# Kernel tuning notes

Hardware: AMD Instinct MI355X
Metric: run time of the kernel (lower is better)

The kernel has to match this reference:

```python
import jax, jax.numpy as jnp
import numpy as np

N_CLASSES_FG = 20  # n_classes - 1

def _norm(t, axis=1):
    # F.normalize(t, dim=axis, eps=1e-10)
    n = jnp.linalg.norm(t, axis=axis, keepdims=True)
    return t / jnp.maximum(n, 1e-10)

def setup_inputs() -> dict:
    key = jax.random.key(0)
    ks = jax.random.split(key, 6)
    B, C, H, W = 8, 512, 80, 80
    N, Hr, Wr = 100, 40, 40
    return {
        "code_C": jax.random.normal(ks[0], (B, C, H, W), jnp.float32),
        "code_BG": jax.random.normal(ks[1], (B, C, H, W), jnp.float32),
        "ref_code_c": jax.random.normal(ks[2], (N, C, Hr, Wr), jnp.float32),
        "ref_code_bg": jax.random.normal(ks[3], (N, C, Hr, Wr), jnp.float32),
        "sum_patch_coord": jax.random.randint(ks[4], (N, 2), 0, Hr, dtype=jnp.int32),
        "cls_mask": jax.random.randint(ks[5], (N,), 0, N_CLASSES_FG, dtype=jnp.int32),
    }

def reference(code_C, code_BG, ref_code_c, ref_code_bg, sum_patch_coord, cls_mask):
    B, Cdim, H, W = code_C.shape
    N = ref_code_c.shape[0]
    code_C = _norm(code_C)   # channelwise L2 normalize
    code_BG = _norm(code_BG)
    # gather per-annotation feature vectors: ref_code_c[i, :, pc[i,1], pc[i,0]] -> [N, C]
    code_vectors = ref_code_c[jnp.arange(N), :, sum_patch_coord[:, 1], sum_patch_coord[:, 0]]
    # mean-mode prototypes: class-wise mean of gathered vectors
    protos = jax.ops.segment_sum(code_vectors, cls_mask, num_segments=N_CLASSES_FG)  # [V, C]
    counts = jax.ops.segment_sum(jnp.ones((N,), code_vectors.dtype), cls_mask, num_segments=N_CLASSES_FG)
    protos = protos / jnp.maximum(counts, 1.0)[:, None]  # classes with 0 vectors stay zero
    # cosine-similarity maps against normalized prototypes
    prob_C = jnp.einsum('bchw,vc->bvhw', code_C, _norm(protos, axis=1))  # [B, V, H, W]
    # pick the most-background pixel (min of summed class similarity), k=1 topk(-x)
    flat = prob_C.sum(axis=1).reshape(B, -1)  # [B, H*W]
    idx = jnp.argmin(flat, axis=1)
    i_x, i_y = idx // W, idx % W
    min_vec = code_BG[jnp.arange(B), :, i_x, i_y]  # [B, C]
    prob_BG = jnp.einsum('bchw,bc->bhw', code_BG, min_vec)  # [B, H, W]
    probs = jnp.concatenate([prob_BG[:, None], prob_C], axis=1)  # [B, V+1, H, W]
    return jax.nn.softmax(probs, axis=1)
```

## Files before the change

### kernel.cpp

```cpp
#include <hip/hip_runtime.h>
#include <math.h>

#define BB 8
#define CC 512
#define HWSZ 6400
#define NN 100
#define HR 40
#define WR 40
#define VV 20
#define VO 21
#define TPX 256
#define NT (HWSZ / TPX)

typedef unsigned long long u64;

__device__ __forceinline__ unsigned mapf(float f) {
    unsigned b = __float_as_uint(f);
    return (b & 0x80000000u) ? ~b : (b | 0x80000000u);
}

__global__ __launch_bounds__(512) void k_protos(const float* __restrict__ refc,
                                                const int* __restrict__ coord,
                                                const int* __restrict__ cls,
                                                float* __restrict__ protosT,
                                                u64* __restrict__ batchMin) {
    const int v = blockIdx.x;
    const int c = threadIdx.x;
    if (v == 0 && c < BB) batchMin[c] = ~0ull;

    float acc = 0.f;
    int cnt = 0;
    for (int n = 0; n < NN; ++n) {
        if (cls[n] == v) {
            int y = coord[2 * n + 1];
            int x = coord[2 * n + 0];
            acc += refc[((size_t)(n * CC + c) * HR + y) * WR + x];
            ++cnt;
        }
    }
    acc /= fmaxf((float)cnt, 1.0f);

    float ss = acc * acc;
    #pragma unroll
    for (int off = 32; off; off >>= 1) ss += __shfl_xor(ss, off);
    __shared__ float sW[8];
    const int wave = c >> 6, lane = c & 63;
    if (lane == 0) sW[wave] = ss;
    __syncthreads();
    float tot = 0.f;
    #pragma unroll
    for (int w = 0; w < 8; ++w) tot += sW[w];
    float scale = 1.0f / fmaxf(sqrtf(tot), 1e-10f);

    protosT[c * VV + v] = acc * scale;
}

__global__ __launch_bounds__(256) void k_probC_part(const float* __restrict__ codeC,
                                                    const float* __restrict__ protosT,
                                                    float* __restrict__ partC) {
    __shared__ float red[4 * 11 * TPX];

    const int tid  = threadIdx.x;
    const int w    = tid >> 6, lane = tid & 63;
    const int blk  = blockIdx.x;
    const int cg   = blk & 1;
    const int tile = (blk >> 1) % NT;
    const int b    = blk / (2 * NT);
    const int c0   = __builtin_amdgcn_readfirstlane(cg * 256 + w * 64);

    const float* src = codeC + ((size_t)(b * CC + c0)) * HWSZ + tile * TPX + 4 * lane;
    const float* pt  = protosT + (size_t)c0 * VV;

    float4 d[VV];
    #pragma unroll
    for (int v = 0; v < VV; ++v) d[v] = make_float4(0.f, 0.f, 0.f, 0.f);
    float4 ss = make_float4(0.f, 0.f, 0.f, 0.f);

    #pragma unroll 8
    for (int c = 0; c < 64; ++c) {
        float4 x = *(const float4*)(src + (size_t)c * HWSZ);
        ss.x = fmaf(x.x, x.x, ss.x);
        ss.y = fmaf(x.y, x.y, ss.y);
        ss.z = fmaf(x.z, x.z, ss.z);
        ss.w = fmaf(x.w, x.w, ss.w);
        const float* pr = pt + c * VV;
        #pragma unroll
        for (int v = 0; v < VV; ++v) {
            float p = pr[v];
            d[v].x = fmaf(x.x, p, d[v].x);
            d[v].y = fmaf(x.y, p, d[v].y);
            d[v].z = fmaf(x.z, p, d[v].z);
            d[v].w = fmaf(x.w, p, d[v].w);
        }
    }

    float* dstp = partC + (size_t)blk * (VO * TPX);

    *(float4*)&red[(w * 11 + 0) * TPX + 4 * lane] = ss;
    #pragma unroll
    for (int r = 0; r < 10; ++r)
        *(float4*)&red[(w * 11 + 1 + r) * TPX + 4 * lane] = d[r];
    __syncthreads();
    for (int q = tid; q < 11 * TPX; q += 256) {
        float t = red[q] + red[11 * TPX + q] + red[22 * TPX + q] + red[33 * TPX + q];
        dstp[q] = t;
    }
    __syncthreads();

    #pragma unroll
    for (int r = 0; r < 10; ++r)
        *(float4*)&red[(w * 11 + r) * TPX + 4 * lane] = d[10 + r];
    __syncthreads();
    for (int q = tid; q < 10 * TPX; q += 256) {
        float t = red[q] + red[11 * TPX + q] + red[22 * TPX + q] + red[33 * TPX + q];
        dstp[11 * TPX + q] = t;
    }
}

__global__ __launch_bounds__(256) void k_finishC(const float* __restrict__ partC,
                                                 float* __restrict__ probC,
                                                 u64* __restrict__ batchMin) {
    __shared__ u64 sKey[4];
    const int tid  = threadIdx.x;
    const int tile = blockIdx.x % NT;
    const int b    = blockIdx.x / NT;

    const float* p0 = partC + ((size_t)(b * 2 * NT + tile * 2)) * (VO * TPX);
    const float* p1 = p0 + VO * TPX;

    float ssT = p0[tid] + p1[tid];
    float scale = 1.0f / fmaxf(sqrtf(ssT), 1e-10f);

    float psum = 0.f;
    float* dst = probC + (size_t)b * VV * HWSZ + tile * TPX;
    #pragma unroll
    for (int v = 0; v < VV; ++v) {
        float dv = p0[(1 + v) * TPX + tid] + p1[(1 + v) * TPX + tid];
        float pv = dv * scale;
        dst[(size_t)v * HWSZ + tid] = pv;
        psum += pv;
    }

    u64 key = ((u64)mapf(psum) << 32) | (unsigned)(tile * TPX + tid);
    #pragma unroll
    for (int off = 32; off; off >>= 1) {
        u64 o = __shfl_xor(key, off);
        if (o < key) key = o;
    }
    if ((tid & 63) == 0) sKey[tid >> 6] = key;
    __syncthreads();
    if (tid == 0) {
        u64 kk = sKey[0];
        kk = sKey[1] < kk ? sKey[1] : kk;
        kk = sKey[2] < kk ? sKey[2] : kk;
        kk = sKey[3] < kk ? sKey[3] : kk;
        atomicMin(&batchMin[b], kk);
    }
}

__global__ __launch_bounds__(512) void k_minvec(const u64* __restrict__ batchMin,
                                                const float* __restrict__ codeBG,
                                                float* __restrict__ minvecN) {
    const int b = blockIdx.x, c = threadIdx.x;
    const int pix = (int)(unsigned)(batchMin[b] & 0xFFFFFFFFull);
    float x = codeBG[(size_t)(b * CC + c) * HWSZ + pix];
    float ss = x * x;
    #pragma unroll
    for (int off = 32; off; off >>= 1) ss += __shfl_xor(ss, off);
    __shared__ float sW[8];
    if ((c & 63) == 0) sW[c >> 6] = ss;
    __syncthreads();
    float tot = 0.f;
    #pragma unroll
    for (int w = 0; w < 8; ++w) tot += sW[w];
    minvecN[b * CC + c] = x * (1.0f / fmaxf(sqrtf(tot), 1e-10f));
}

__global__ __launch_bounds__(256) void k_bg_part(const float* __restrict__ codeBG,
                                                 const float* __restrict__ minvecN,
                                                 float* __restrict__ partBG) {
    __shared__ float red[4 * 2 * TPX];

    const int tid  = threadIdx.x;
    const int w    = tid >> 6, lane = tid & 63;
    const int blk  = blockIdx.x;
    const int cg   = blk & 1;
    const int tile = (blk >> 1) % NT;
    const int b    = blk / (2 * NT);
    const int c0   = __builtin_amdgcn_readfirstlane(cg * 256 + w * 64);

    const float* src = codeBG + ((size_t)(b * CC + c0)) * HWSZ + tile * TPX + 4 * lane;
    const float* mv  = minvecN + b * CC + c0;

    float4 ss = make_float4(0.f, 0.f, 0.f, 0.f);
    float4 dg = make_float4(0.f, 0.f, 0.f, 0.f);

    #pragma unroll 8
    for (int c = 0; c < 64; ++c) {
        float4 x = *(const float4*)(src + (size_t)c * HWSZ);
        float m = mv[c];
        ss.x = fmaf(x.x, x.x, ss.x);
        ss.y = fmaf(x.y, x.y, ss.y);
        ss.z = fmaf(x.z, x.z, ss.z);
        ss.w = fmaf(x.w, x.w, ss.w);
        dg.x = fmaf(x.x, m, dg.x);
        dg.y = fmaf(x.y, m, dg.y);
        dg.z = fmaf(x.z, m, dg.z);
        dg.w = fmaf(x.w, m, dg.w);
    }

    *(float4*)&red[(w * 2 + 0) * TPX + 4 * lane] = ss;
    *(float4*)&red[(w * 2 + 1) * TPX + 4 * lane] = dg;
    __syncthreads();

    float* dstp = partBG + (size_t)blk * (2 * TPX);
    for (int q = tid; q < 2 * TPX; q += 256) {
        float t = red[q] + red[2 * TPX + q] + red[4 * TPX + q] + red[6 * TPX + q];
        dstp[q] = t;
    }
}

__global__ __launch_bounds__(256) void k_finishBG(const float* __restrict__ partBG,
                                                  const float* __restrict__ probC,
                                                  float* __restrict__ out) {
    const int tid  = threadIdx.x;
    const int tile = blockIdx.x % NT;
    const int b    = blockIdx.x / NT;

    const float* q0 = partBG + ((size_t)(b * 2 * NT + tile * 2)) * (2 * TPX);
    const float* q1 = q0 + 2 * TPX;

    float ssT = q0[tid] + q1[tid];
    float dgT = q0[TPX + tid] + q1[TPX + tid];
    float pbg = dgT * (1.0f / fmaxf(sqrtf(ssT), 1e-10f));

    float pv[VO];
    pv[0] = pbg;
    const float* pc = probC + (size_t)b * VV * HWSZ + tile * TPX + tid;
    #pragma unroll
    for (int v = 0; v < VV; ++v) pv[v + 1] = pc[(size_t)v * HWSZ];

    float m = pv[0];
    #pragma unroll
    for (int i = 1; i < VO; ++i) m = fmaxf(m, pv[i]);
    float se = 0.f;
    #pragma unroll
    for (int i = 0; i < VO; ++i) { pv[i] = __expf(pv[i] - m); se += pv[i]; }
    float inv = 1.0f / se;

    float* dstp = out + (size_t)b * VO * HWSZ + tile * TPX + tid;
    #pragma unroll
    for (int i = 0; i < VO; ++i) dstp[(size_t)i * HWSZ] = pv[i] * inv;
}

extern "C" void kernel_launch(void* const* d_in, const int* in_sizes, int n_in,
                              void* d_out, int out_size, void* d_ws, size_t ws_size,
                              hipStream_t stream) {
    const float* codeC  = (const float*)d_in[0];
    const float* codeBG = (const float*)d_in[1];
    const float* refc   = (const float*)d_in[2];
    const int* coord = (const int*)d_in[4];
    const int* cls   = (const int*)d_in[5];
    float* out = (float*)d_out;

    char* ws = (char*)d_ws;
    float* protosT  = (float*)(ws);
    float* probC    = (float*)(ws + 40960);
    float* minvecN  = (float*)(ws + 4136960);
    u64*   batchMin = (u64*)  (ws + 4153344);
    float* partC    = (float*)(ws + 4153408);
    float* partBG   = (float*)(ws + 12755008);

    k_protos    <<<dim3(VV),          dim3(512), 0, stream>>>(refc, coord, cls, protosT, batchMin);
    k_probC_part<<<dim3(BB * NT * 2), dim3(256), 0, stream>>>(codeC, protosT, partC);
    k_finishC   <<<dim3(BB * NT),     dim3(256), 0, stream>>>(partC, probC, batchMin);
    k_minvec    <<<dim3(BB),          dim3(512), 0, stream>>>(batchMin, codeBG, minvecN);
    k_bg_part   <<<dim3(BB * NT * 2), dim3(256), 0, stream>>>(codeBG, minvecN, partBG);
    k_finishBG  <<<dim3(BB * NT),     dim3(256), 0, stream>>>(partBG, probC, out);
}
```

Before: 67.60 us.

## Fuse finish stages into partial kernels via last-block atomic counters

Merges the six launches into three. The last of the two channel-group blocks per tile finishes the tile, and the last tile per batch computes the normalized min vector, all coordinated through atomic counters and thread fences. This removes launch gaps and the separate small kernels that run at low occupancy. In exchange it adds fences, atomics and serialized tail work inside the big kernels, and the counters must be reset by k_protos on each call.

```diff
diff --git a/kernel.cpp b/kernel.cpp
--- a/kernel.cpp
+++ b/kernel.cpp
@@ -23,10 +23,16 @@
                                                 const int* __restrict__ coord,
                                                 const int* __restrict__ cls,
                                                 float* __restrict__ protosT,
-                                                u64* __restrict__ batchMin) {
+                                                u64* __restrict__ batchMin,
+                                                unsigned* __restrict__ tileCntA,
+                                                unsigned* __restrict__ tileCntB,
+                                                unsigned* __restrict__ batchCnt) {
     const int v = blockIdx.x;
     const int c = threadIdx.x;
-    if (v == 0 && c < BB) batchMin[c] = ~0ull;
+    if (v == 0) {
+        if (c < BB * NT) { tileCntA[c] = 0u; tileCntB[c] = 0u; }
+        if (c < BB) { batchCnt[c] = 0u; batchMin[c] = ~0ull; }
+    }
 
     float acc = 0.f;
     int cnt = 0;
@@ -55,10 +61,20 @@
     protosT[c * VV + v] = acc * scale;
 }
 
-__global__ __launch_bounds__(256) void k_probC_part(const float* __restrict__ codeC,
-                                                    const float* __restrict__ protosT,
-                                                    float* __restrict__ partC) {
+__global__ __launch_bounds__(256) void k_probC(const float* __restrict__ codeC,
+                                               const float* __restrict__ codeBG,
+                                               const float* __restrict__ protosT,
+                                               float* __restrict__ partC,
+                                               float* __restrict__ probC,
+                                               u64* __restrict__ batchMin,
+                                               unsigned* __restrict__ tileCntA,
+                                               unsigned* __restrict__ batchCnt,
+                                               float* __restrict__ minvecN) {
     __shared__ float red[4 * 11 * TPX];
+    __shared__ u64 sKey[4];
+    __shared__ int sLast, sBLast;
+    __shared__ unsigned sPix;
+    __shared__ float sR[4];
 
     const int tid  = threadIdx.x;
     const int w    = tid >> 6, lane = tid & 63;
@@ -115,22 +131,21 @@
         float t = red[q] + red[11 * TPX + q] + red[22 * TPX + q] + red[33 * TPX + q];
         dstp[11 * TPX + q] = t;
     }
-}
-
-__global__ __launch_bounds__(256) void k_finishC(const float* __restrict__ partC,
-                                                 float* __restrict__ probC,
-                                                 u64* __restrict__ batchMin) {
-    __shared__ u64 sKey[4];
-    const int tid  = threadIdx.x;
-    const int tile = blockIdx.x % NT;
-    const int b    = blockIdx.x / NT;
-
-    const float* p0 = partC + ((size_t)(b * 2 * NT + tile * 2)) * (VO * TPX);
+
+    __threadfence();
+    if (tid == 0) {
+        unsigned old = atomicAdd(&tileCntA[b * NT + tile], 1u);
+        sLast = (old == 1u) ? 1 : 0;
+    }
+    __syncthreads();
+    if (!sLast) return;
+    __threadfence();
+
+    const float* p0 = partC + (size_t)(b * 2 * NT + tile * 2) * (VO * TPX);
     const float* p1 = p0 + VO * TPX;
 
     float ssT = p0[tid] + p1[tid];
     float scale = 1.0f / fmaxf(sqrtf(ssT), 1e-10f);
-
     float psum = 0.f;
     float* dst = probC + (size_t)b * VV * HWSZ + tile * TPX;
     #pragma unroll
@@ -147,7 +162,7 @@
         u64 o = __shfl_xor(key, off);
         if (o < key) key = o;
     }
-    if ((tid & 63) == 0) sKey[tid >> 6] = key;
+    if (lane == 0) sKey[w] = key;
     __syncthreads();
     if (tid == 0) {
         u64 kk = sKey[0];
@@ -155,31 +170,41 @@
         kk = sKey[2] < kk ? sKey[2] : kk;
         kk = sKey[3] < kk ? sKey[3] : kk;
         atomicMin(&batchMin[b], kk);
-    }
-}
-
-__global__ __launch_bounds__(512) void k_minvec(const u64* __restrict__ batchMin,
-                                                const float* __restrict__ codeBG,
-                                                float* __restrict__ minvecN) {
-    const int b = blockIdx.x, c = threadIdx.x;
-    const int pix = (int)(unsigned)(batchMin[b] & 0xFFFFFFFFull);
-    float x = codeBG[(size_t)(b * CC + c) * HWSZ + pix];
-    float ss = x * x;
-    #pragma unroll
-    for (int off = 32; off; off >>= 1) ss += __shfl_xor(ss, off);
-    __shared__ float sW[8];
-    if ((c & 63) == 0) sW[c >> 6] = ss;
-    __syncthreads();
-    float tot = 0.f;
-    #pragma unroll
-    for (int w = 0; w < 8; ++w) tot += sW[w];
-    minvecN[b * CC + c] = x * (1.0f / fmaxf(sqrtf(tot), 1e-10f));
-}
-
-__global__ __launch_bounds__(256) void k_bg_part(const float* __restrict__ codeBG,
-                                                 const float* __restrict__ minvecN,
-                                                 float* __restrict__ partBG) {
+        __threadfence();
+        unsigned old = atomicAdd(&batchCnt[b], 1u);
+        sBLast = (old == NT - 1) ? 1 : 0;
+    }
+    __syncthreads();
+
+    if (!sBLast) return;
+    if (tid == 0) {
+        __threadfence();
+        u64 kk = atomicMin(&batchMin[b], ~0ull);
+        sPix = (unsigned)(kk & 0xFFFFFFFFull);
+    }
+    __syncthreads();
+    const int pix = (int)sPix;
+    float x0 = codeBG[((size_t)(b * CC + tid)) * HWSZ + pix];
+    float x1 = codeBG[((size_t)(b * CC + 256 + tid)) * HWSZ + pix];
+    float s2 = fmaf(x0, x0, x1 * x1);
+    #pragma unroll
+    for (int off = 32; off; off >>= 1) s2 += __shfl_xor(s2, off);
+    if (lane == 0) sR[w] = s2;
+    __syncthreads();
+    float totq = sR[0] + sR[1] + sR[2] + sR[3];
+    float sc = 1.0f / fmaxf(sqrtf(totq), 1e-10f);
+    minvecN[b * CC + tid] = x0 * sc;
+    minvecN[b * CC + 256 + tid] = x1 * sc;
+}
+
+__global__ __launch_bounds__(256) void k_bg(const float* __restrict__ codeBG,
+                                            const float* __restrict__ minvecN,
+                                            const float* __restrict__ probC,
+                                            float* __restrict__ partBG,
+                                            unsigned* __restrict__ tileCntB,
+                                            float* __restrict__ out) {
     __shared__ float red[4 * 2 * TPX];
+    __shared__ int sLast;
 
     const int tid  = threadIdx.x;
     const int w    = tid >> 6, lane = tid & 63;
@@ -218,16 +243,17 @@
         float t = red[q] + red[2 * TPX + q] + red[4 * TPX + q] + red[6 * TPX + q];
         dstp[q] = t;
     }
-}
-
-__global__ __launch_bounds__(256) void k_finishBG(const float* __restrict__ partBG,
-                                                  const float* __restrict__ probC,
-                                                  float* __restrict__ out) {
-    const int tid  = threadIdx.x;
-    const int tile = blockIdx.x % NT;
-    const int b    = blockIdx.x / NT;
-
-    const float* q0 = partBG + ((size_t)(b * 2 * NT + tile * 2)) * (2 * TPX);
+
+    __threadfence();
+    if (tid == 0) {
+        unsigned old = atomicAdd(&tileCntB[b * NT + tile], 1u);
+        sLast = (old == 1u) ? 1 : 0;
+    }
+    __syncthreads();
+    if (!sLast) return;
+    __threadfence();
+
+    const float* q0 = partBG + (size_t)(b * 2 * NT + tile * 2) * (2 * TPX);
     const float* q1 = q0 + 2 * TPX;
 
     float ssT = q0[tid] + q1[tid];
@@ -248,9 +274,9 @@
     for (int i = 0; i < VO; ++i) { pv[i] = __expf(pv[i] - m); se += pv[i]; }
     float inv = 1.0f / se;
 
-    float* dstp = out + (size_t)b * VO * HWSZ + tile * TPX + tid;
-    #pragma unroll
-    for (int i = 0; i < VO; ++i) dstp[(size_t)i * HWSZ] = pv[i] * inv;
+    float* dstq = out + (size_t)b * VO * HWSZ + tile * TPX + tid;
+    #pragma unroll
+    for (int i = 0; i < VO; ++i) dstq[(size_t)i * HWSZ] = pv[i] * inv;
 }
 
 extern "C" void kernel_launch(void* const* d_in, const int* in_sizes, int n_in,
@@ -264,17 +290,20 @@
     float* out = (float*)d_out;
 
     char* ws = (char*)d_ws;
-    float* protosT  = (float*)(ws);
-    float* probC    = (float*)(ws + 40960);
-    float* minvecN  = (float*)(ws + 4136960);
-    u64*   batchMin = (u64*)  (ws + 4153344);
-    float* partC    = (float*)(ws + 4153408);
-    float* partBG   = (float*)(ws + 12755008);
-
-    k_protos    <<<dim3(VV),          dim3(512), 0, stream>>>(refc, coord, cls, protosT, batchMin);
-    k_probC_part<<<dim3(BB * NT * 2), dim3(256), 0, stream>>>(codeC, protosT, partC);
-    k_finishC   <<<dim3(BB * NT),     dim3(256), 0, stream>>>(partC, probC, batchMin);
-    k_minvec    <<<dim3(BB),          dim3(512), 0, stream>>>(batchMin, codeBG, minvecN);
-    k_bg_part   <<<dim3(BB * NT * 2), dim3(256), 0, stream>>>(codeBG, minvecN, partBG);
-    k_finishBG  <<<dim3(BB * NT),     dim3(256), 0, stream>>>(partBG, probC, out);
-}
+    float*    protosT  = (float*)   (ws);
+    float*    probC    = (float*)   (ws + 40960);
+    float*    minvecN  = (float*)   (ws + 4136960);
+    u64*      batchMin = (u64*)     (ws + 4153344);
+    unsigned* tileCntA = (unsigned*)(ws + 4153408);
+    unsigned* tileCntB = (unsigned*)(ws + 4154208);
+    unsigned* batchCnt = (unsigned*)(ws + 4155008);
+    float*    partC    = (float*)   (ws + 4160000);
+    float*    partBG   = (float*)   (ws + 12761600);
+
+    k_protos<<<dim3(VV),          dim3(512), 0, stream>>>(refc, coord, cls, protosT,
+                                                          batchMin, tileCntA, tileCntB, batchCnt);
+    k_probC <<<dim3(BB * NT * 2), dim3(256), 0, stream>>>(codeC, codeBG, protosT, partC, probC,
+                                                          batchMin, tileCntA, batchCnt, minvecN);
+    k_bg    <<<dim3(BB * NT * 2), dim3(256), 0, stream>>>(codeBG, minvecN, probC, partBG,
+                                                          tileCntB, out);
+}
```

After: 217.8 us. 222% more time.

## Fuse min-vector extraction into finishC via last-block atomic counter

Applied to the files above, without the earlier changes.

Removes the separate k_minvec launch. The last block per batch to finish k_finishC, found with a per-batch atomic counter and threadfence, reads the selected background pixel vector and normalizes it. k_protos also becomes branchless with an unrolled loop, so gathers are issued unconditionally and loads gain ILP. This saves one kernel launch and its dependency gap, but adds an atomic and a serialized tail in the last block, and k_protos now does 100 gathers per thread instead of about 5.

```diff
diff --git a/kernel.cpp b/kernel.cpp
--- a/kernel.cpp
+++ b/kernel.cpp
@@ -23,20 +23,23 @@
                                                 const int* __restrict__ coord,
                                                 const int* __restrict__ cls,
                                                 float* __restrict__ protosT,
-                                                u64* __restrict__ batchMin) {
+                                                u64* __restrict__ batchMin,
+                                                unsigned* __restrict__ batchCnt) {
     const int v = blockIdx.x;
     const int c = threadIdx.x;
-    if (v == 0 && c < BB) batchMin[c] = ~0ull;
+    if (v == 0 && c < BB) { batchMin[c] = ~0ull; batchCnt[c] = 0u; }
 
     float acc = 0.f;
     int cnt = 0;
+    #pragma unroll 10
     for (int n = 0; n < NN; ++n) {
-        if (cls[n] == v) {
-            int y = coord[2 * n + 1];
-            int x = coord[2 * n + 0];
-            acc += refc[((size_t)(n * CC + c) * HR + y) * WR + x];
-            ++cnt;
-        }
+        int cm = cls[n];
+        int y = coord[2 * n + 1];
+        int x = coord[2 * n + 0];
+        float val = refc[((size_t)(n * CC + c) * HR + y) * WR + x];
+        bool take = (cm == v);
+        acc += take ? val : 0.f;
+        cnt += take ? 1 : 0;
     }
     acc /= fmaxf((float)cnt, 1.0f);
 
@@ -118,10 +121,18 @@
 }
 
 __global__ __launch_bounds__(256) void k_finishC(const float* __restrict__ partC,
+                                                 const float* __restrict__ codeBG,
                                                  float* __restrict__ probC,
-                                                 u64* __restrict__ batchMin) {
+                                                 u64* __restrict__ batchMin,
+                                                 unsigned* __restrict__ batchCnt,
+                                                 float* __restrict__ minvecN) {
     __shared__ u64 sKey[4];
-    const int tid  = threadIdx.x;
+    __shared__ int sBLast;
+    __shared__ unsigned sPix;
+    __shared__ float sR[4];
+
+    const int tid  = threadIdx.x;
+    const int lane = tid & 63, w = tid >> 6;
     const int tile = blockIdx.x % NT;
     const int b    = blockIdx.x / NT;
 
@@ -147,7 +158,7 @@
         u64 o = __shfl_xor(key, off);
         if (o < key) key = o;
     }
-    if ((tid & 63) == 0) sKey[tid >> 6] = key;
+    if (lane == 0) sKey[w] = key;
     __syncthreads();
     if (tid == 0) {
         u64 kk = sKey[0];
@@ -155,25 +166,31 @@
         kk = sKey[2] < kk ? sKey[2] : kk;
         kk = sKey[3] < kk ? sKey[3] : kk;
         atomicMin(&batchMin[b], kk);
-    }
-}
-
-__global__ __launch_bounds__(512) void k_minvec(const u64* __restrict__ batchMin,
-                                                const float* __restrict__ codeBG,
-                                                float* __restrict__ minvecN) {
-    const int b = blockIdx.x, c = threadIdx.x;
-    const int pix = (int)(unsigned)(batchMin[b] & 0xFFFFFFFFull);
-    float x = codeBG[(size_t)(b * CC + c) * HWSZ + pix];
-    float ss = x * x;
-    #pragma unroll
-    for (int off = 32; off; off >>= 1) ss += __shfl_xor(ss, off);
-    __shared__ float sW[8];
-    if ((c & 63) == 0) sW[c >> 6] = ss;
-    __syncthreads();
-    float tot = 0.f;
-    #pragma unroll
-    for (int w = 0; w < 8; ++w) tot += sW[w];
-    minvecN[b * CC + c] = x * (1.0f / fmaxf(sqrtf(tot), 1e-10f));
+        __threadfence();
+        unsigned old = atomicAdd(&batchCnt[b], 1u);
+        sBLast = (old == NT - 1) ? 1 : 0;
+    }
+    __syncthreads();
+
+    if (!sBLast) return;
+    if (tid == 0) {
+        __threadfence();
+        u64 kk = atomicMin(&batchMin[b], ~0ull);
+        sPix = (unsigned)(kk & 0xFFFFFFFFull);
+    }
+    __syncthreads();
+    const int pix = (int)sPix;
+    float x0 = codeBG[((size_t)(b * CC + tid)) * HWSZ + pix];
+    float x1 = codeBG[((size_t)(b * CC + 256 + tid)) * HWSZ + pix];
+    float s2 = fmaf(x0, x0, x1 * x1);
+    #pragma unroll
+    for (int off = 32; off; off >>= 1) s2 += __shfl_xor(s2, off);
+    if (lane == 0) sR[w] = s2;
+    __syncthreads();
+    float totq = sR[0] + sR[1] + sR[2] + sR[3];
+    float sc = 1.0f / fmaxf(sqrtf(totq), 1e-10f);
+    minvecN[b * CC + tid] = x0 * sc;
+    minvecN[b * CC + 256 + tid] = x1 * sc;
 }
 
 __global__ __launch_bounds__(256) void k_bg_part(const float* __restrict__ codeBG,
@@ -264,17 +281,19 @@
     float* out = (float*)d_out;
 
     char* ws = (char*)d_ws;
-    float* protosT  = (float*)(ws);
-    float* probC    = (float*)(ws + 40960);
-    float* minvecN  = (float*)(ws + 4136960);
-    u64*   batchMin = (u64*)  (ws + 4153344);
-    float* partC    = (float*)(ws + 4153408);
-    float* partBG   = (float*)(ws + 12755008);
-
-    k_protos    <<<dim3(VV),          dim3(512), 0, stream>>>(refc, coord, cls, protosT, batchMin);
+    float*    protosT  = (float*)   (ws);
+    float*    probC    = (float*)   (ws + 40960);
+    float*    minvecN  = (float*)   (ws + 4136960);
+    u64*      batchMin = (u64*)     (ws + 4153344);
+    unsigned* batchCnt = (unsigned*)(ws + 4153408);
+    float*    partC    = (float*)   (ws + 4153472);
+    float*    partBG   = (float*)   (ws + 12755072);
+
+    k_protos    <<<dim3(VV),          dim3(512), 0, stream>>>(refc, coord, cls, protosT,
+                                                              batchMin, batchCnt);
     k_probC_part<<<dim3(BB * NT * 2), dim3(256), 0, stream>>>(codeC, protosT, partC);
-    k_finishC   <<<dim3(BB * NT),     dim3(256), 0, stream>>>(partC, probC, batchMin);
-    k_minvec    <<<dim3(BB),          dim3(512), 0, stream>>>(batchMin, codeBG, minvecN);
+    k_finishC   <<<dim3(BB * NT),     dim3(256), 0, stream>>>(partC, codeBG, probC,
+                                                              batchMin, batchCnt, minvecN);
     k_bg_part   <<<dim3(BB * NT * 2), dim3(256), 0, stream>>>(codeBG, minvecN, partBG);
     k_finishBG  <<<dim3(BB * NT),     dim3(256), 0, stream>>>(partBG, probC, out);
 }
```

New measurement: 116.7 us. 1.73x slower.
